# Performance work log

Hardware: AMD Instinct MI355X
Metric: run time of the kernel (lower is better)

Reference implementation:

```python
import jax, jax.numpy as jnp
import numpy as np

GRID_SIZE = 5
SPLINE_ORDER = 3

def _grid(in_features, dtype):
    # efficient-KAN default grid over [-1, 1], extended by spline_order knots each side
    h = 2.0 / GRID_SIZE
    g = jnp.arange(-SPLINE_ORDER, GRID_SIZE + SPLINE_ORDER + 1, dtype=dtype) * h - 1.0
    return jnp.broadcast_to(g, (in_features, g.shape[0]))  # (in, G+2k+1)

def _b_splines(x, grid):
    # x: (..., in) -> bases: (..., in, G+k) via Cox-de Boor recursion
    xk = x[..., None]
    bases = ((xk >= grid[:, :-1]) & (xk < grid[:, 1:])).astype(x.dtype)
    for k in range(1, SPLINE_ORDER + 1):
        left = (xk - grid[:, :-(k + 1)]) / (grid[:, k:-1] - grid[:, :-(k + 1)]) * bases[..., :-1]
        right = (grid[:, k + 1:] - xk) / (grid[:, k + 1:] - grid[:, 1:-k]) * bases[..., 1:]
        bases = left + right
    return bases

def _kan_linear(x, base_w, spline_w, scaler):
    # base branch: SiLU(x) @ W_base^T ; spline branch: einsum over B-spline basis
    grid = _grid(base_w.shape[1], x.dtype)
    bases = _b_splines(x, grid)                      # (..., in, G+k)
    scaled = spline_w * scaler[..., None]            # (out, in, G+k)
    base_out = jax.nn.silu(x) @ base_w.T
    spline_out = jnp.einsum('...ig,oig->...o', bases, scaled)
    return base_out + spline_out

def setup_inputs() -> dict:
    key = jax.random.key(0)
    ks = jax.random.split(key, 11)
    B, N, C, O = 2, 256, 64, 64
    GK = GRID_SIZE + SPLINE_ORDER
    return {
        'x': jax.random.normal(ks[0], (B, N, C), jnp.float32),
        'adj': jax.random.randint(ks[1], (B, N, N), 0, 2, jnp.int32),
        'fw_base': jax.random.normal(ks[2], (1, C), jnp.float32) * 0.1,
        'fw_spline': jax.random.normal(ks[3], (1, C, GK), jnp.float32) * 0.1,
        'fw_scaler': jax.random.normal(ks[4], (1, C), jnp.float32) * 0.1,
        'mw_base': jax.random.normal(ks[5], (O, C), jnp.float32) * 0.1,
        'mw_spline': jax.random.normal(ks[6], (O, C, GK), jnp.float32) * 0.1,
        'mw_scaler': jax.random.normal(ks[7], (O, C), jnp.float32) * 0.1,
        'uw_base': jax.random.normal(ks[8], (O, C + O), jnp.float32) * 0.1,
        'uw_spline': jax.random.normal(ks[9], (O, C + O, GK), jnp.float32) * 0.1,
        'uw_scaler': jax.random.normal(ks[10], (O, C + O), jnp.float32) * 0.1,
    }

def reference(x, adj, fw_base, fw_spline, fw_scaler, mw_base, mw_spline, mw_scaler, uw_base, uw_spline, uw_scaler):
    # r_ij = h_i - h_j : (B, N, N, C)
    r_ij = x[:, :, None, :] - x[:, None, :, :]
    energy = _kan_linear(r_ij, fw_base, fw_spline, fw_scaler)[..., 0]  # (B, N, N)
    energy = jnp.where(adj == 0, jnp.asarray(-1e9, energy.dtype), energy)
    alpha = jax.nn.softmax(energy, axis=-1)
    msg_val = _kan_linear(x, mw_base, mw_spline, mw_scaler)            # (B, N, O)
    aggr = jnp.einsum('bij,bjo->bio', alpha, msg_val)
    combined = jnp.concatenate([x, aggr], axis=-1)
    return _kan_linear(combined, uw_base, uw_spline, uw_scaler)
```

## Files before the change

kernel.cpp:

```cpp
#include <hip/hip_runtime.h>
#include <math.h>

#define NB 256
#define CH 64
#define OUTF 64
#define GK 8
#define UIN 128

#define WS_MSG 0
#define WS_CPAD 32768
#define WS_XT 36864

__device__ __forceinline__ float silu(float v) {
    return v * __builtin_amdgcn_rcpf(1.0f + __expf(-v));
}

__device__ __forceinline__ void spline4(float r, int& d, float4& v) {
    float p = (r + 2.2f) * 2.5f;
    float fd = floorf(p);
    d = (int)fd;
    float u = p - fd;
    if ((unsigned)d > 10u) d = 11;
    float um = 1.0f - u;
    float u2 = u * u, u3 = u2 * u;
    const float k6 = 1.0f / 6.0f;
    v.x = um * um * um * k6;
    v.y = (3.0f * u3 - 6.0f * u2 + 4.0f) * k6;
    v.z = (-3.0f * u3 + 3.0f * u2 + 3.0f * u + 1.0f) * k6;
    v.w = u3 * k6;
}

template <int W>
__device__ __forceinline__ void basis_col(float v, float (*Bt)[W], int c) {
    int d; float4 vv; spline4(v, d, vv);
#pragma unroll
    for (int g = 0; g < 8; ++g) Bt[g][c] = 0.0f;
#pragma unroll
    for (int k = 0; k < 4; ++k) {
        int m = d - 3 + k;
        if ((unsigned)m < 8u) Bt[m][c] = ((const float*)&vv)[k];
    }
    Bt[8][c] = silu(v);
}

__global__ __launch_bounds__(256, 2) void msg_prep_kernel(
    const float* __restrict__ x,
    const float* __restrict__ fws, const float* __restrict__ fwsc,
    const float* __restrict__ mwb, const float* __restrict__ mws,
    const float* __restrict__ mwsc,
    float* __restrict__ ws) {
    const int blk = blockIdx.x, tid = threadIdx.x;

    if (blk >= 513) {
        __shared__ float tile[64][65];
        const int blk2 = blk - 513, b = blk2 >> 2, jt = blk2 & 3;
#pragma unroll
        for (int it = 0; it < 16; ++it) {
            int idx = it * 256 + tid, jj = idx >> 6, cc = idx & 63;
            tile[jj][cc] = x[(b * NB + jt * 64 + jj) * CH + cc];
        }
        __syncthreads();
#pragma unroll
        for (int it = 0; it < 16; ++it) {
            int idx = it * 256 + tid, cc = idx >> 6, jj = idx & 63;
            ws[WS_XT + b * CH * NB + cc * NB + jt * 64 + jj] = tile[jj][cc];
        }
        return;
    }
    if (blk == 512) {
        for (int e = tid; e < CH * 16; e += 256) {
            int c = e >> 4, dd = e & 15;
            float4 cf = make_float4(0.f, 0.f, 0.f, 0.f);
            if (dd <= 10) {
                float sc = fwsc[c];
                float w0 = 0.f, w1 = 0.f, w2 = 0.f, w3 = 0.f;
                int m0 = dd - 3;
                if ((unsigned)(m0 + 0) < 8u) w0 = fws[c * GK + m0 + 0] * sc;
                if ((unsigned)(m0 + 1) < 8u) w1 = fws[c * GK + m0 + 1] * sc;
                if ((unsigned)(m0 + 2) < 8u) w2 = fws[c * GK + m0 + 2] * sc;
                if ((unsigned)(m0 + 3) < 8u) w3 = fws[c * GK + m0 + 3] * sc;
                cf.x = (w0 + 4.0f * w1 + w2) * (1.0f / 6.0f);
                cf.y = (w2 - w0) * 0.5f;
                cf.z = (w0 - 2.0f * w1 + w2) * 0.5f;
                cf.w = (w3 - w0 + 3.0f * (w1 - w2)) * (1.0f / 6.0f);
            }
            ((float4*)(ws + WS_CPAD))[e] = cf;
        }
        return;
    }

    const int row = blk, lane = tid & 63, w = tid >> 6;
    __shared__ float Bt[9][CH];
    if (tid < CH) basis_col<CH>(x[row * CH + tid], Bt, tid);
    __syncthreads();

    float B[9];
#pragma unroll
    for (int g = 0; g < 9; ++g) B[g] = Bt[g][lane];

    float outv = 0.0f;
#pragma unroll 4
    for (int oi = 0; oi < 16; ++oi) {
        int o = w * 16 + oi;
        const float4* wp = (const float4*)&mws[(o * CH + lane) * GK];
        float4 wa = wp[0], wb4 = wp[1];
        float sc = mwsc[o * CH + lane];
        float bw = mwb[o * CH + lane];
        float val = (B[0]*wa.x + B[1]*wa.y + B[2]*wa.z + B[3]*wa.w
                   + B[4]*wb4.x + B[5]*wb4.y + B[6]*wb4.z + B[7]*wb4.w) * sc
                  + B[8] * bw;
#pragma unroll
        for (int off = 32; off > 0; off >>= 1) val += __shfl_xor(val, off, 64);
        if (lane == oi) outv = val;
    }
    if (lane < 16) ws[WS_MSG + row * OUTF + w * 16 + lane] = outv;
}

__global__ __launch_bounds__(256, 2) void gat_kernel(
    const float* __restrict__ x, const int* __restrict__ adj,
    const float* __restrict__ fwb,
    const float* __restrict__ uwb, const float* __restrict__ uws,
    const float* __restrict__ uwsc,
    const float* __restrict__ ws, float* __restrict__ out) {
    const int b = blockIdx.x >> 8, i = blockIdx.x & 255;
    const int tid = threadIdx.x, lane = tid & 63, w = tid >> 6;

    __shared__ float4 cpad[CH][16];
    __shared__ float2 xisf[CH];
    __shared__ float alpha[NB];
    __shared__ float Bt[9][UIN];
    __shared__ float part[4][OUTF];
    __shared__ float wred[4];

    {
        const float4* cp = (const float4*)(ws + WS_CPAD);
        float4* dst = &cpad[0][0];
        for (int e = tid; e < CH * 16; e += 256) dst[e] = cp[e];
    }
    if (tid < CH) {
        float v = x[(b * NB + i) * CH + tid];
        xisf[tid] = make_float2(v, fwb[tid]);
        basis_col<UIN>(v, Bt, tid);
    }
    __syncthreads();

    float msgv[64];
    const float* msgb = ws + WS_MSG + (b * NB + w * 64) * OUTF + lane;
#pragma unroll
    for (int jj = 0; jj < 64; ++jj) msgv[jj] = msgb[jj * OUTF];
    const int av = adj[(b * NB + i) * NB + tid];

    const float* xTb = ws + WS_XT + b * CH * NB;
    float e = 0.0f;
#pragma unroll 8
    for (int c = 0; c < CH; ++c) {
        float xj = xTb[c * NB + tid];
        float2 xs = xisf[c];
        float r = xs.x - xj;
        float pp = (r + 2.2f) * 2.5f;
        float fd = floorf(pp);
        int d = (int)fd;
        float u = pp - fd;
        if ((unsigned)d > 10u) d = 11;
        float4 cf = cpad[c][d];
        e += cf.x + u * (cf.y + u * (cf.z + u * cf.w)) + silu(r) * xs.y;
    }
    float pexp = av ? __expf(e) : 0.0f;
    alpha[tid] = pexp;
    float sw = pexp;
#pragma unroll
    for (int off = 32; off > 0; off >>= 1) sw += __shfl_xor(sw, off, 64);
    if (lane == 0) wred[w] = sw;
    __syncthreads();

    float rden = __builtin_amdgcn_rcpf(wred[0] + wred[1] + wred[2] + wred[3]);

    {
        float a = 0.0f;
#pragma unroll
        for (int jj = 0; jj < 64; ++jj)
            a += alpha[w * 64 + jj] * msgv[jj];
        part[w][lane] = a;
    }
    __syncthreads();

    if (tid < OUTF) {
        float ag = (part[0][tid] + part[1][tid] + part[2][tid] + part[3][tid])
                 * rden;
        basis_col<UIN>(ag, Bt, CH + tid);
    }
    __syncthreads();

    float BA[9], BB[9];
#pragma unroll
    for (int g = 0; g < 9; ++g) {
        BA[g] = Bt[g][2 * lane];
        BB[g] = Bt[g][2 * lane + 1];
    }
    float outv = 0.0f;
#pragma unroll 4
    for (int oi = 0; oi < 16; ++oi) {
        int o = w * 16 + oi;
        const float4* wp = (const float4*)&uws[(o * UIN + 2 * lane) * GK];
        float4 a0 = wp[0], a1 = wp[1], b0 = wp[2], b1 = wp[3];
        float2 sc2 = *(const float2*)&uwsc[o * UIN + 2 * lane];
        float2 bw2 = *(const float2*)&uwb[o * UIN + 2 * lane];
        float sA = BA[0]*a0.x + BA[1]*a0.y + BA[2]*a0.z + BA[3]*a0.w
                 + BA[4]*a1.x + BA[5]*a1.y + BA[6]*a1.z + BA[7]*a1.w;
        float sB = BB[0]*b0.x + BB[1]*b0.y + BB[2]*b0.z + BB[3]*b0.w
                 + BB[4]*b1.x + BB[5]*b1.y + BB[6]*b1.z + BB[7]*b1.w;
        float val = sA * sc2.x + BA[8] * bw2.x + sB * sc2.y + BB[8] * bw2.y;
#pragma unroll
        for (int off = 32; off > 0; off >>= 1) val += __shfl_xor(val, off, 64);
        if (lane == oi) outv = val;
    }
    if (lane < 16) out[(b * NB + i) * OUTF + w * 16 + lane] = outv;
}

extern "C" void kernel_launch(void* const* d_in, const int* in_sizes, int n_in,
                              void* d_out, int out_size, void* d_ws, size_t ws_size,
                              hipStream_t stream) {
    const float* x     = (const float*)d_in[0];
    const int*   adj   = (const int*)d_in[1];
    const float* fwb   = (const float*)d_in[2];
    const float* fws   = (const float*)d_in[3];
    const float* fwsc  = (const float*)d_in[4];
    const float* mwb   = (const float*)d_in[5];
    const float* mws   = (const float*)d_in[6];
    const float* mwsc  = (const float*)d_in[7];
    const float* uwb   = (const float*)d_in[8];
    const float* uws   = (const float*)d_in[9];
    const float* uwsc  = (const float*)d_in[10];
    float* out = (float*)d_out;
    float* ws = (float*)d_ws;

    msg_prep_kernel<<<521, 256, 0, stream>>>(x, fws, fwsc, mwb, mws, mwsc, ws);
    gat_kernel<<<512, 256, 0, stream>>>(x, adj, fwb, uwb, uws, uwsc, ws, out);
}
```

Baseline: 120.4 us.

## Move energy computation into first kernel with finer-grained blocks and coalesced weight loads

The pairwise energy/softmax-numerator computation moves out of the second kernel into the first. There it is split into 2048 blocks, one per (row, 64-column tile), with the x tile transposed in shared memory and the spline coefficients built per block. Unnormalized exponentials and partial sums go to the workspace, and the second kernel only aggregates and applies the update KAN. Weight loads in both KAN matvecs are reorganized so consecutive lanes read consecutive float4s. This raises parallelism and occupancy for the dominant O(N^2·C) part, at the cost of redundant coefficient setup per block and an extra workspace round trip for the exponentials.

After: 121.7 us. No clear change (+1.1%).

```diff
diff --git a/kernel.cpp b/kernel.cpp
--- a/kernel.cpp
+++ b/kernel.cpp
@@ -8,8 +8,8 @@
 #define UIN 128
 
 #define WS_MSG 0
-#define WS_CPAD 32768
-#define WS_XT 36864
+#define WS_PEXP 32768
+#define WS_PSUM 163840
 
 __device__ __forceinline__ float silu(float v) {
     return v * __builtin_amdgcn_rcpf(1.0f + __expf(-v));
@@ -43,147 +43,162 @@
     Bt[8][c] = silu(v);
 }
 
-__global__ __launch_bounds__(256, 2) void msg_prep_kernel(
-    const float* __restrict__ x,
-    const float* __restrict__ fws, const float* __restrict__ fwsc,
+__global__ __launch_bounds__(256, 4) void k1_kernel(
+    const float* __restrict__ x, const int* __restrict__ adj,
+    const float* __restrict__ fwb, const float* __restrict__ fws,
+    const float* __restrict__ fwsc,
     const float* __restrict__ mwb, const float* __restrict__ mws,
     const float* __restrict__ mwsc,
     float* __restrict__ ws) {
     const int blk = blockIdx.x, tid = threadIdx.x;
-
-    if (blk >= 513) {
-        __shared__ float tile[64][65];
-        const int blk2 = blk - 513, b = blk2 >> 2, jt = blk2 & 3;
-#pragma unroll
-        for (int it = 0; it < 16; ++it) {
-            int idx = it * 256 + tid, jj = idx >> 6, cc = idx & 63;
-            tile[jj][cc] = x[(b * NB + jt * 64 + jj) * CH + cc];
-        }
+    const int lane = tid & 63, w = tid >> 6;
+
+    __shared__ union {
+        float mBt[9][CH];
+        struct {
+            float tile[CH][65];
+            __align__(16) float4 cpad[CH][12];
+            float2 xisf[CH];
+            float part[4][64];
+        } e;
+    } sm;
+
+    if (blk < 512) {
+        const int row = blk;
+        if (tid < CH) basis_col<CH>(x[row * CH + tid], sm.mBt, tid);
         __syncthreads();
-#pragma unroll
-        for (int it = 0; it < 16; ++it) {
-            int idx = it * 256 + tid, cc = idx >> 6, jj = idx & 63;
-            ws[WS_XT + b * CH * NB + cc * NB + jt * 64 + jj] = tile[jj][cc];
-        }
+
+        const int c1 = lane >> 1, c2 = c1 + 32, gs = (lane & 1) * 4;
+        float B1[4], B2[4];
+#pragma unroll
+        for (int k = 0; k < 4; ++k) {
+            B1[k] = sm.mBt[gs + k][c1];
+            B2[k] = sm.mBt[gs + k][c2];
+        }
+        float sil1 = sm.mBt[8][c1], sil2 = sm.mBt[8][c2];
+        float bflag = (lane & 1) ? 0.0f : 1.0f;
+
+        float outv = 0.0f;
+#pragma unroll 4
+        for (int oi = 0; oi < 16; ++oi) {
+            int o = w * 16 + oi;
+            const float4* wp = (const float4*)(mws + o * CH * GK);
+            float4 wA = wp[lane];
+            float4 wB = wp[64 + lane];
+            float scA = mwsc[o * CH + c1], scB = mwsc[o * CH + c2];
+            float bwA = mwb[o * CH + c1], bwB = mwb[o * CH + c2];
+            float val = (B1[0]*wA.x + B1[1]*wA.y + B1[2]*wA.z + B1[3]*wA.w) * scA
+                      + (B2[0]*wB.x + B2[1]*wB.y + B2[2]*wB.z + B2[3]*wB.w) * scB
+                      + (sil1 * bwA + sil2 * bwB) * bflag;
+#pragma unroll
+            for (int off = 32; off > 0; off >>= 1)
+                val += __shfl_xor(val, off, 64);
+            if (lane == oi) outv = val;
+        }
+        if (lane < 16) ws[WS_MSG + row * OUTF + w * 16 + lane] = outv;
         return;
     }
-    if (blk == 512) {
-        for (int e = tid; e < CH * 16; e += 256) {
-            int c = e >> 4, dd = e & 15;
-            float4 cf = make_float4(0.f, 0.f, 0.f, 0.f);
-            if (dd <= 10) {
-                float sc = fwsc[c];
-                float w0 = 0.f, w1 = 0.f, w2 = 0.f, w3 = 0.f;
-                int m0 = dd - 3;
-                if ((unsigned)(m0 + 0) < 8u) w0 = fws[c * GK + m0 + 0] * sc;
-                if ((unsigned)(m0 + 1) < 8u) w1 = fws[c * GK + m0 + 1] * sc;
-                if ((unsigned)(m0 + 2) < 8u) w2 = fws[c * GK + m0 + 2] * sc;
-                if ((unsigned)(m0 + 3) < 8u) w3 = fws[c * GK + m0 + 3] * sc;
-                cf.x = (w0 + 4.0f * w1 + w2) * (1.0f / 6.0f);
-                cf.y = (w2 - w0) * 0.5f;
-                cf.z = (w0 - 2.0f * w1 + w2) * 0.5f;
-                cf.w = (w3 - w0 + 3.0f * (w1 - w2)) * (1.0f / 6.0f);
-            }
-            ((float4*)(ws + WS_CPAD))[e] = cf;
-        }
-        return;
-    }
-
-    const int row = blk, lane = tid & 63, w = tid >> 6;
-    __shared__ float Bt[9][CH];
-    if (tid < CH) basis_col<CH>(x[row * CH + tid], Bt, tid);
-    __syncthreads();
-
-    float B[9];
-#pragma unroll
-    for (int g = 0; g < 9; ++g) B[g] = Bt[g][lane];
-
-    float outv = 0.0f;
-#pragma unroll 4
-    for (int oi = 0; oi < 16; ++oi) {
-        int o = w * 16 + oi;
-        const float4* wp = (const float4*)&mws[(o * CH + lane) * GK];
-        float4 wa = wp[0], wb4 = wp[1];
-        float sc = mwsc[o * CH + lane];
-        float bw = mwb[o * CH + lane];
-        float val = (B[0]*wa.x + B[1]*wa.y + B[2]*wa.z + B[3]*wa.w
-                   + B[4]*wb4.x + B[5]*wb4.y + B[6]*wb4.z + B[7]*wb4.w) * sc
-                  + B[8] * bw;
-#pragma unroll
-        for (int off = 32; off > 0; off >>= 1) val += __shfl_xor(val, off, 64);
-        if (lane == oi) outv = val;
-    }
-    if (lane < 16) ws[WS_MSG + row * OUTF + w * 16 + lane] = outv;
-}
-
-__global__ __launch_bounds__(256, 2) void gat_kernel(
-    const float* __restrict__ x, const int* __restrict__ adj,
-    const float* __restrict__ fwb,
-    const float* __restrict__ uwb, const float* __restrict__ uws,
-    const float* __restrict__ uwsc,
-    const float* __restrict__ ws, float* __restrict__ out) {
-    const int b = blockIdx.x >> 8, i = blockIdx.x & 255;
-    const int tid = threadIdx.x, lane = tid & 63, w = tid >> 6;
-
-    __shared__ float4 cpad[CH][16];
-    __shared__ float2 xisf[CH];
-    __shared__ float alpha[NB];
-    __shared__ float Bt[9][UIN];
-    __shared__ float part[4][OUTF];
-    __shared__ float wred[4];
+
+    const int eb = blk - 512;
+    const int b = eb >> 10, rem = eb & 1023, i = rem >> 2, jt = rem & 3;
 
     {
-        const float4* cp = (const float4*)(ws + WS_CPAD);
-        float4* dst = &cpad[0][0];
-        for (int e = tid; e < CH * 16; e += 256) dst[e] = cp[e];
-    }
-    if (tid < CH) {
-        float v = x[(b * NB + i) * CH + tid];
-        xisf[tid] = make_float2(v, fwb[tid]);
-        basis_col<UIN>(v, Bt, tid);
-    }
-    __syncthreads();
-
-    float msgv[64];
-    const float* msgb = ws + WS_MSG + (b * NB + w * 64) * OUTF + lane;
-#pragma unroll
-    for (int jj = 0; jj < 64; ++jj) msgv[jj] = msgb[jj * OUTF];
-    const int av = adj[(b * NB + i) * NB + tid];
-
-    const float* xTb = ws + WS_XT + b * CH * NB;
+        const float* xb = x + (b * NB + jt * 64) * CH;
+#pragma unroll
+        for (int k = 0; k < 4; ++k) {
+            int f = k * 1024 + tid * 4;
+            float4 v = *(const float4*)(xb + f);
+            int j = f >> 6, c = f & 63;
+            sm.e.tile[c + 0][j] = v.x;
+            sm.e.tile[c + 1][j] = v.y;
+            sm.e.tile[c + 2][j] = v.z;
+            sm.e.tile[c + 3][j] = v.w;
+        }
+    }
+#pragma unroll
+    for (int ee = tid; ee < CH * 12; ee += 256) {
+        int c = ee / 12, dd = ee - c * 12;
+        float4 cf = make_float4(0.f, 0.f, 0.f, 0.f);
+        if (dd <= 10) {
+            float sc = fwsc[c];
+            float w0 = 0.f, w1 = 0.f, w2 = 0.f, w3 = 0.f;
+            int m0 = dd - 3;
+            if ((unsigned)(m0 + 0) < 8u) w0 = fws[c * GK + m0 + 0] * sc;
+            if ((unsigned)(m0 + 1) < 8u) w1 = fws[c * GK + m0 + 1] * sc;
+            if ((unsigned)(m0 + 2) < 8u) w2 = fws[c * GK + m0 + 2] * sc;
+            if ((unsigned)(m0 + 3) < 8u) w3 = fws[c * GK + m0 + 3] * sc;
+            cf.x = (w0 + 4.0f * w1 + w2) * (1.0f / 6.0f);
+            cf.y = (w2 - w0) * 0.5f;
+            cf.z = (w0 - 2.0f * w1 + w2) * 0.5f;
+            cf.w = (w3 - w0 + 3.0f * (w1 - w2)) * (1.0f / 6.0f);
+        }
+        sm.e.cpad[c][dd] = cf;
+    }
+    if (tid < CH)
+        sm.e.xisf[tid] = make_float2(x[(b * NB + i) * CH + tid], fwb[tid]);
+    __syncthreads();
+
+    const int j = lane, c0 = w * 16;
     float e = 0.0f;
-#pragma unroll 8
-    for (int c = 0; c < CH; ++c) {
-        float xj = xTb[c * NB + tid];
-        float2 xs = xisf[c];
+#pragma unroll
+    for (int cc = 0; cc < 16; ++cc) {
+        int c = c0 + cc;
+        float xj = sm.e.tile[c][j];
+        float2 xs = sm.e.xisf[c];
         float r = xs.x - xj;
         float pp = (r + 2.2f) * 2.5f;
         float fd = floorf(pp);
         int d = (int)fd;
         float u = pp - fd;
         if ((unsigned)d > 10u) d = 11;
-        float4 cf = cpad[c][d];
+        float4 cf = sm.e.cpad[c][d];
         e += cf.x + u * (cf.y + u * (cf.z + u * cf.w)) + silu(r) * xs.y;
     }
-    float pexp = av ? __expf(e) : 0.0f;
-    alpha[tid] = pexp;
-    float sw = pexp;
-#pragma unroll
-    for (int off = 32; off > 0; off >>= 1) sw += __shfl_xor(sw, off, 64);
-    if (lane == 0) wred[w] = sw;
-    __syncthreads();
-
-    float rden = __builtin_amdgcn_rcpf(wred[0] + wred[1] + wred[2] + wred[3]);
+    sm.e.part[w][j] = e;
+    __syncthreads();
+
+    if (tid < 64) {
+        float et = sm.e.part[0][tid] + sm.e.part[1][tid]
+                 + sm.e.part[2][tid] + sm.e.part[3][tid];
+        int av = adj[(b * NB + i) * NB + jt * 64 + tid];
+        float pe = av ? __expf(et) : 0.0f;
+        ws[WS_PEXP + (b * NB + i) * NB + jt * 64 + tid] = pe;
+        float sw = pe;
+#pragma unroll
+        for (int off = 32; off > 0; off >>= 1)
+            sw += __shfl_xor(sw, off, 64);
+        if (tid == 0) ws[WS_PSUM + ((b * NB + i) << 2) + jt] = sw;
+    }
+}
+
+__global__ __launch_bounds__(256, 4) void k2_kernel(
+    const float* __restrict__ x,
+    const float* __restrict__ uwb, const float* __restrict__ uws,
+    const float* __restrict__ uwsc,
+    const float* __restrict__ ws, float* __restrict__ out) {
+    const int b = blockIdx.x >> 8, i = blockIdx.x & 255;
+    const int tid = threadIdx.x, lane = tid & 63, w = tid >> 6;
+
+    __shared__ float p[NB];
+    __shared__ float Bt[9][UIN];
+    __shared__ float part[4][OUTF];
+
+    p[tid] = ws[WS_PEXP + (b * NB + i) * NB + tid];
+    if (tid < CH)
+        basis_col<UIN>(x[(b * NB + i) * CH + tid], Bt, tid);
+    const float* ps = ws + WS_PSUM + ((b * NB + i) << 2);
+    float rden = __builtin_amdgcn_rcpf(ps[0] + ps[1] + ps[2] + ps[3]);
+    __syncthreads();
 
     {
+        const float* msgb = ws + WS_MSG + (b * NB + w * 64) * OUTF + lane;
         float a = 0.0f;
-#pragma unroll
+#pragma unroll 8
         for (int jj = 0; jj < 64; ++jj)
-            a += alpha[w * 64 + jj] * msgv[jj];
+            a += p[w * 64 + jj] * msgb[jj * OUTF];
         part[w][lane] = a;
     }
     __syncthreads();
-
     if (tid < OUTF) {
         float ag = (part[0][tid] + part[1][tid] + part[2][tid] + part[3][tid])
                  * rden;
@@ -191,27 +206,39 @@
     }
     __syncthreads();
 
-    float BA[9], BB[9];
-#pragma unroll
-    for (int g = 0; g < 9; ++g) {
-        BA[g] = Bt[g][2 * lane];
-        BB[g] = Bt[g][2 * lane + 1];
-    }
+    const int c1 = lane >> 1, gs = (lane & 1) * 4;
+    float B1[4], B2[4], B3[4], B4[4];
+#pragma unroll
+    for (int k = 0; k < 4; ++k) {
+        B1[k] = Bt[gs + k][c1];
+        B2[k] = Bt[gs + k][c1 + 32];
+        B3[k] = Bt[gs + k][c1 + 64];
+        B4[k] = Bt[gs + k][c1 + 96];
+    }
+    float s1 = Bt[8][c1], s2 = Bt[8][c1 + 32];
+    float s3 = Bt[8][c1 + 64], s4 = Bt[8][c1 + 96];
+    float bflag = (lane & 1) ? 0.0f : 1.0f;
+
     float outv = 0.0f;
-#pragma unroll 4
+#pragma unroll 2
     for (int oi = 0; oi < 16; ++oi) {
         int o = w * 16 + oi;
-        const float4* wp = (const float4*)&uws[(o * UIN + 2 * lane) * GK];
-        float4 a0 = wp[0], a1 = wp[1], b0 = wp[2], b1 = wp[3];
-        float2 sc2 = *(const float2*)&uwsc[o * UIN + 2 * lane];
-        float2 bw2 = *(const float2*)&uwb[o * UIN + 2 * lane];
-        float sA = BA[0]*a0.x + BA[1]*a0.y + BA[2]*a0.z + BA[3]*a0.w
-                 + BA[4]*a1.x + BA[5]*a1.y + BA[6]*a1.z + BA[7]*a1.w;
-        float sB = BB[0]*b0.x + BB[1]*b0.y + BB[2]*b0.z + BB[3]*b0.w
-                 + BB[4]*b1.x + BB[5]*b1.y + BB[6]*b1.z + BB[7]*b1.w;
-        float val = sA * sc2.x + BA[8] * bw2.x + sB * sc2.y + BB[8] * bw2.y;
-#pragma unroll
-        for (int off = 32; off > 0; off >>= 1) val += __shfl_xor(val, off, 64);
+        const float4* wp = (const float4*)(uws + o * UIN * GK);
+        float4 w1 = wp[lane];
+        float4 w2 = wp[64 + lane];
+        float4 w3 = wp[128 + lane];
+        float4 w4 = wp[192 + lane];
+        const float* scp = uwsc + o * UIN;
+        const float* bwp = uwb + o * UIN;
+        float val = (B1[0]*w1.x + B1[1]*w1.y + B1[2]*w1.z + B1[3]*w1.w) * scp[c1]
+                  + (B2[0]*w2.x + B2[1]*w2.y + B2[2]*w2.z + B2[3]*w2.w) * scp[c1 + 32]
+                  + (B3[0]*w3.x + B3[1]*w3.y + B3[2]*w3.z + B3[3]*w3.w) * scp[c1 + 64]
+                  + (B4[0]*w4.x + B4[1]*w4.y + B4[2]*w4.z + B4[3]*w4.w) * scp[c1 + 96]
+                  + (s1 * bwp[c1] + s2 * bwp[c1 + 32]
+                   + s3 * bwp[c1 + 64] + s4 * bwp[c1 + 96]) * bflag;
+#pragma unroll
+        for (int off = 32; off > 0; off >>= 1)
+            val += __shfl_xor(val, off, 64);
         if (lane == oi) outv = val;
     }
     if (lane < 16) out[(b * NB + i) * OUTF + w * 16 + lane] = outv;
@@ -234,6 +261,7 @@
     float* out = (float*)d_out;
     float* ws = (float*)d_ws;
 
-    msg_prep_kernel<<<521, 256, 0, stream>>>(x, fws, fwsc, mwb, mws, mwsc, ws);
-    gat_kernel<<<512, 256, 0, stream>>>(x, adj, fwb, uwb, uws, uwsc, ws, out);
-}
+    k1_kernel<<<2560, 256, 0, stream>>>(x, adj, fwb, fws, fwsc,
+                                        mwb, mws, mwsc, ws);
+    k2_kernel<<<512, 256, 0, stream>>>(x, uwb, uws, uwsc, ws, out);
+}
```
